# Kernel tuning notes

Hardware: AMD Instinct MI355X
Metric: run time of the kernel (lower is better)

Reference implementation:

```python
import jax, jax.numpy as jnp
import numpy as np
from jax import lax

B, N, S = 4, 16384, 4096
D1, D2 = 128, 256
MLP = (256, 128)
EPS_W = 1e-8
EPS_BN = 1e-5
BIG = 1e8


def setup_inputs() -> dict:
    key = jax.random.key(0)
    ks = jax.random.split(key, 10)
    inp = {
        "xyz1": jax.random.normal(ks[0], (B, 3, N), jnp.float32),
        "xyz2": jax.random.normal(ks[1], (B, 3, S), jnp.float32),
        "points1": jax.random.normal(ks[2], (B, D1, N), jnp.float32),
        "points2": jax.random.normal(ks[3], (B, D2, S), jnp.float32),
        "idx1": jnp.repeat(jnp.arange(B, dtype=jnp.int32), N).reshape(B, N),
        "idx2": jnp.repeat(jnp.arange(B, dtype=jnp.int32), S).reshape(B, S),
    }
    cin = D1 + D2
    inp["w1"] = jax.random.normal(ks[4], (MLP[0], cin), jnp.float32) * 0.05
    inp["b1"] = jnp.zeros((MLP[0],), jnp.float32)
    inp["g1"] = jnp.ones((MLP[0],), jnp.float32)
    inp["be1"] = jnp.zeros((MLP[0],), jnp.float32)
    inp["w2"] = jax.random.normal(ks[5], (MLP[1], MLP[0]), jnp.float32) * 0.05
    inp["b2"] = jnp.zeros((MLP[1],), jnp.float32)
    inp["g2"] = jnp.ones((MLP[1],), jnp.float32)
    inp["be2"] = jnp.zeros((MLP[1],), jnp.float32)
    return inp


def _bn_relu(x, gamma, beta):
    # training-mode batchnorm over (B, N) per channel, then relu; x: [B, C, N]
    mean = jnp.mean(x, axis=(0, 2), keepdims=True)
    var = jnp.var(x, axis=(0, 2), keepdims=True)  # biased, as torch BN
    xn = (x - mean) * lax.rsqrt(var + EPS_BN)
    return jax.nn.relu(xn * gamma[None, :, None] + beta[None, :, None])


def _fp_forward(xyz1, xyz2, points1, points2, idx1, idx2,
                w1, b1, g1, be1, w2, b2, g2, be2):
    x1 = jnp.transpose(xyz1, (0, 2, 1))  # [B, N, 3]
    x2 = jnp.transpose(xyz2, (0, 2, 1))  # [B, S, 3]
    p2 = jnp.transpose(points2, (0, 2, 1))  # [B, S, D2]

    # squared pairwise distances [B, N, S]
    d = -2.0 * jnp.einsum('bnc,bsc->bns', x1, x2)
    d = d + jnp.sum(x1 * x1, -1)[:, :, None] + jnp.sum(x2 * x2, -1)[:, None, :]
    d = jnp.where(idx1[:, :, None] == idx2[:, None, :], d, jnp.inf)

    # 3 nearest neighbors (top-k on negated distances == sort-ascending take 3)
    neg_d3, idx3 = lax.top_k(-d, 3)          # [B, N, 3]
    d3 = -neg_d3
    recip = 1.0 / (d3 + EPS_W)
    weight = recip / jnp.sum(recip, axis=2, keepdims=True)
    weight = jnp.where(d3 > BIG, 0.0, weight)
    weight = jnp.nan_to_num(weight)

    gathered = jax.vmap(lambda p, i: p[i])(p2, idx3)   # [B, N, 3, D2]
    interp = jnp.sum(gathered * weight[..., None], axis=2)  # [B, N, D2]

    newp = jnp.concatenate([jnp.transpose(points1, (0, 2, 1)), interp], axis=-1)
    newp = jnp.transpose(newp, (0, 2, 1))  # [B, D1+D2, N]

    # 1x1 conv -> BN -> relu, twice
    h = jnp.einsum('bcn,oc->bon', newp, w1) + b1[None, :, None]
    h = _bn_relu(h, g1, be1)
    h = jnp.einsum('bcn,oc->bon', h, w2) + b2[None, :, None]
    h = _bn_relu(h, g2, be2)
    return h


def reference(xyz1, xyz2, points1, points2, idx1, idx2,
              w1, b1, g1, be1, w2, b2, g2, be2):
    return _fp_forward(xyz1, xyz2, points1, points2, idx1, idx2,
                       w1, b1, g1, be1, w2, b2, g2, be2)
```

## Files before the change

kernel.cpp:

```cpp
#include <hip/hip_runtime.h>
#include <hip/hip_bf16.h>

#define INF_F (__builtin_inff())

typedef __attribute__((ext_vector_type(8))) short bf16x8;
typedef __attribute__((ext_vector_type(4))) float f32x4;

__device__ __forceinline__ unsigned short f2bf(float f) {
  __hip_bfloat16 h = __float2bfloat16(f);
  return __builtin_bit_cast(unsigned short, h);
}
__device__ __forceinline__ float bf2f(unsigned short u) {
  return __uint_as_float((unsigned)u << 16);
}

#define TOP3_INS(d, sj, E0, E1, E2, J0, J1, J2)                      \
  {                                                                  \
    bool l0 = (d) < E0, l1 = (d) < E1;                               \
    E2 = l1 ? E1 : (d); J2 = l1 ? J1 : (sj);                         \
    E1 = l0 ? E0 : (l1 ? (d) : E1); J1 = l0 ? J0 : (l1 ? (sj) : J1); \
    E0 = l0 ? (d) : E0; J0 = l0 ? (sj) : J0;                         \
  }


__global__ __launch_bounds__(256) void prep_k(const float* __restrict__ p2,
                                              const float* __restrict__ p1,
                                              const float* __restrict__ w1,
                                              const float* __restrict__ w2,
                                              const float* __restrict__ xyz2,
                                              const int* __restrict__ idx1,
                                              const int* __restrict__ idx2,
                                              unsigned short* __restrict__ p2t,
                                              unsigned short* __restrict__ X,
                                              unsigned short* __restrict__ w1b,
                                              unsigned short* __restrict__ w2b,
                                              float4* __restrict__ pack,
                                              float* __restrict__ stats) {
  int id = blockIdx.x;
  int t = threadIdx.x;
  if (id < 4096) {
    __shared__ float tile[32][33];
    int s0 = (id & 127) * 32;
    int k0 = ((id >> 7) & 7) * 32;
    int b = id >> 10;
    int tx = t & 31, ty = t >> 5;
    const float* src = p2 + ((size_t)b * 256 + k0) * 4096 + s0;
    for (int r = ty; r < 32; r += 8) tile[r][tx] = src[(size_t)r * 4096 + tx];
    __syncthreads();
    unsigned short* dst = p2t + ((size_t)b * 4096 + s0) * 256 + k0;
    for (int r = ty; r < 32; r += 8) dst[(size_t)r * 256 + tx] = f2bf(tile[tx][r]);
  } else if (id < 12288) {
    __shared__ float tile[32][33];
    int id2 = id - 4096;
    int n0 = (id2 & 511) * 32;
    int c0 = ((id2 >> 9) & 3) * 32;
    int b = id2 >> 11;
    int tx = t & 31, ty = t >> 5;
    const float* src = p1 + ((size_t)b * 128 + c0) * 16384 + n0;
    for (int r = ty; r < 32; r += 8) tile[r][tx] = src[(size_t)r * 16384 + tx];
    __syncthreads();
    for (int r = ty; r < 32; r += 8)
      X[((size_t)(b * 16384 + n0 + r)) * 384 + c0 + tx] = f2bf(tile[tx][r]);
  } else if (id < 12864) {
    int id3 = (id - 12288) * 256 + t;
    if (id3 < 98304) {
      w1b[id3] = f2bf(w1[id3]);
    } else if (id3 < 131072) {
      w2b[id3 - 98304] = f2bf(w2[id3 - 98304]);
    } else {
      int pid = id3 - 131072;
      int b = pid >> 12, s = pid & 4095;
      float x = xyz2[(b * 3 + 0) * 4096 + s];
      float y = xyz2[(b * 3 + 1) * 4096 + s];
      float z = xyz2[(b * 3 + 2) * 4096 + s];
      float w = fmaf(x, x, fmaf(y, y, z * z));
      int common = idx1[b * 16384];
      w = (idx2[b * 4096 + s] == common) ? w : 3e38f;
      pack[b * 4096 + s] = make_float4(x, y, z, w);
    }
  } else {
    for (int i = t; i < 768; i += 256) stats[i] = 0.f;
  }
}

__global__ __launch_bounds__(256) void knn_k(const float* __restrict__ xyz1,
                                             const float* __restrict__ xyz2,
                                             const int* __restrict__ idx1,
                                             const int* __restrict__ idx2,
                                             const float4* __restrict__ pack,
                                             float* __restrict__ rec) {
  int bid = blockIdx.x;
  int qg = bid >> 3, sl = bid & 7;
  int b = qg >> 6;
  int nloc = (qg & 63) << 8;
  int t = threadIdx.x;
  int n = nloc + t;
  int q0i = b * 16384 + n;
  int common = idx1[b * 16384];
  int sbase = sl << 9;
  const float4* ps = pack + b * 4096 + sbase;
  float px = xyz1[(b * 3 + 0) * 16384 + n];
  float py = xyz1[(b * 3 + 1) * 16384 + n];
  float pz = xyz1[(b * 3 + 2) * 16384 + n];
  int myid = idx1[q0i];
  float pn = fmaf(px, px, fmaf(py, py, pz * pz));
  float qx = -2.f * px, qy = -2.f * py, qz = -2.f * pz;
  float e0 = INF_F, e1 = INF_F, e2 = INF_F;
  int j0 = 0, j1 = 0, j2 = 0;
#pragma unroll 8
  for (int s = 0; s < 512; ++s) {
    float4 p = ps[s];
    float d = fmaf(qx, p.x, fmaf(qy, p.y, fmaf(qz, p.z, pn))) + p.w;
    if (__builtin_expect(d < e2, 0)) {
      int sj = sbase + s;
      TOP3_INS(d, sj, e0, e1, e2, j0, j1, j2);
    }
  }
  if (__builtin_expect(myid != common, 0)) {
    e0 = INF_F; e1 = INF_F; e2 = INF_F; j0 = 0; j1 = 0; j2 = 0;
    for (int s = 0; s < 512; ++s) {
      int gs = sbase + s;
      float x = xyz2[(b * 3 + 0) * 4096 + gs];
      float y = xyz2[(b * 3 + 1) * 4096 + gs];
      float z = xyz2[(b * 3 + 2) * 4096 + gs];
      float w = fmaf(x, x, fmaf(y, y, z * z));
      float d = fmaf(qx, x, fmaf(qy, y, fmaf(qz, z, pn))) + w;
      d = (idx2[b * 4096 + gs] == myid) ? d : INF_F;
      if (d < e2) TOP3_INS(d, gs, e0, e1, e2, j0, j1, j2);
    }
  }
  float* r = &rec[((size_t)sl * 65536 + q0i) * 6];
  r[0] = e0; r[1] = e1; r[2] = e2;
  ((int*)r)[3] = j0; ((int*)r)[4] = j1; ((int*)r)[5] = j2;
}

__global__ __launch_bounds__(256) void interpm_k(const float* __restrict__ rec,
                                                 const unsigned short* __restrict__ p2t,
                                                 unsigned short* __restrict__ X) {
  __shared__ int sId[128][3];
  __shared__ float sWt[128][3];
  int i0 = blockIdx.x * 128;
  int b = i0 >> 14;
  int t = threadIdx.x;
  if (t < 128) {
    int i = i0 + t;
    float e0, e1, e2;
    int j0, j1, j2;
    {
      const float* r = &rec[(size_t)i * 6];
      e0 = r[0]; e1 = r[1]; e2 = r[2];
      j0 = ((const int*)r)[3]; j1 = ((const int*)r)[4]; j2 = ((const int*)r)[5];
    }
#pragma unroll
    for (int c = 1; c < 8; ++c) {
      const float* r = &rec[((size_t)c * 65536 + i) * 6];
      const int* ir = (const int*)r;
#pragma unroll
      for (int w = 0; w < 3; ++w) {
        float d = r[w];
        int sj = ir[3 + w];
        bool l0 = (d < e0) || (d == e0 && sj < j0);
        bool l1 = (d < e1) || (d == e1 && sj < j1);
        bool l2 = (d < e2) || (d == e2 && sj < j2);
        e2 = l1 ? e1 : (l2 ? d : e2);
        j2 = l1 ? j1 : (l2 ? sj : j2);
        e1 = l0 ? e0 : (l1 ? d : e1);
        j1 = l0 ? j0 : (l1 ? sj : j1);
        e0 = l0 ? d : e0;
        j0 = l0 ? sj : j0;
      }
    }
    float r0 = 1.f / (e0 + 1e-8f);
    float r1 = 1.f / (e1 + 1e-8f);
    float r2 = 1.f / (e2 + 1e-8f);
    float rs = r0 + r1 + r2;
    sWt[t][0] = (e0 > 1e8f) ? 0.f : r0 / rs;
    sWt[t][1] = (e1 > 1e8f) ? 0.f : r1 / rs;
    sWt[t][2] = (e2 > 1e8f) ? 0.f : r2 / rs;
    sId[t][0] = j0; sId[t][1] = j1; sId[t][2] = j2;
  }
  __syncthreads();
  int k = t;
  const unsigned short* base = p2t + (size_t)b * 4096 * 256;
#pragma unroll 2
  for (int ii = 0; ii < 128; ++ii) {
    int id0 = sId[ii][0], id1 = sId[ii][1], id2 = sId[ii][2];
    float w0 = sWt[ii][0], w1v = sWt[ii][1], w2v = sWt[ii][2];
    float v = w0 * bf2f(base[id0 * 256 + k]);
    v = fmaf(w1v, bf2f(base[id1 * 256 + k]), v);
    v = fmaf(w2v, bf2f(base[id2 * 256 + k]), v);
    X[(size_t)(i0 + ii) * 384 + 128 + k] = f2bf(v);
  }
}

__global__ __launch_bounds__(256) void gemm1_k(const unsigned short* __restrict__ X,
                                               const unsigned short* __restrict__ Wb,
                                               unsigned short* __restrict__ h1T,
                                               float* __restrict__ stats1) {
  __shared__ unsigned short sW[128][40];
  __shared__ unsigned short sX[128][40];
  int t = threadIdx.x;
  int i0 = blockIdx.x * 128;
  int c0 = blockIdx.y * 128;
  int w = t >> 6, lane = t & 63;
  int wc = (w & 1) * 64, wni = w >> 1;
  int wn = wni * 64;
  int l15 = lane & 15, g = lane >> 4;
  f32x4 acc[4][4];
#pragma unroll
  for (int a = 0; a < 4; ++a)
#pragma unroll
    for (int bq = 0; bq < 4; ++bq) acc[a][bq] = (f32x4)0.f;
  int sr = t & 127, sh = t >> 7;
  for (int kc = 0; kc < 12; ++kc) {
    int k0 = kc * 32;
    __syncthreads();
    {
      const uint4* gw = (const uint4*)&Wb[(size_t)(c0 + sr) * 384 + k0 + sh * 16];
      uint4 v0 = gw[0], v1 = gw[1];
      *(uint4*)&sW[sr][sh * 16] = v0;
      *(uint4*)&sW[sr][sh * 16 + 8] = v1;
      const uint4* gx = (const uint4*)&X[(size_t)(i0 + sr) * 384 + k0 + sh * 16];
      uint4 x0 = gx[0], x1 = gx[1];
      *(uint4*)&sX[sr][sh * 16] = x0;
      *(uint4*)&sX[sr][sh * 16 + 8] = x1;
    }
    __syncthreads();
    bf16x8 a[4], b[4];
#pragma unroll
    for (int tm = 0; tm < 4; ++tm)
      a[tm] = *(const bf16x8*)&sW[wc + tm * 16 + l15][g * 8];
#pragma unroll
    for (int tn = 0; tn < 4; ++tn)
      b[tn] = *(const bf16x8*)&sX[wn + tn * 16 + l15][g * 8];
#pragma unroll
    for (int tm = 0; tm < 4; ++tm)
#pragma unroll
      for (int tn = 0; tn < 4; ++tn)
        acc[tm][tn] = __builtin_amdgcn_mfma_f32_16x16x32_bf16(a[tm], b[tn], acc[tm][tn], 0, 0, 0);
  }
#pragma unroll
  for (int tm = 0; tm < 4; ++tm)
#pragma unroll
    for (int tn = 0; tn < 4; ++tn) {
      int c = c0 + wc + tm * 16 + g * 4;
      int n = i0 + wn + tn * 16 + l15;
      f32x4 v = acc[tm][tn];
      ushort4 o;
      o.x = f2bf(v[0]); o.y = f2bf(v[1]); o.z = f2bf(v[2]); o.w = f2bf(v[3]);
      *(ushort4*)&h1T[(size_t)n * 256 + c] = o;
    }
  float s_[4][4], q_[4][4];
#pragma unroll
  for (int tm = 0; tm < 4; ++tm)
#pragma unroll
    for (int j = 0; j < 4; ++j) {
      float s = 0.f, q = 0.f;
#pragma unroll
      for (int tn = 0; tn < 4; ++tn) {
        float v = acc[tm][tn][j];
        s += v; q = fmaf(v, v, q);
      }
      s_[tm][j] = s; q_[tm][j] = q;
    }
#pragma unroll
  for (int mask = 1; mask < 16; mask <<= 1)
#pragma unroll
    for (int tm = 0; tm < 4; ++tm)
#pragma unroll
      for (int j = 0; j < 4; ++j) {
        s_[tm][j] += __shfl_xor(s_[tm][j], mask);
        q_[tm][j] += __shfl_xor(q_[tm][j], mask);
      }
  __syncthreads();
  float* red = (float*)&sW[0][0];
  if (l15 == 0) {
#pragma unroll
    for (int tm = 0; tm < 4; ++tm)
#pragma unroll
      for (int j = 0; j < 4; ++j) {
        int cl = wc + tm * 16 + g * 4 + j;
        red[(wni * 128 + cl) * 2 + 0] = s_[tm][j];
        red[(wni * 128 + cl) * 2 + 1] = q_[tm][j];
      }
  }
  __syncthreads();
  {
    int cl = t >> 1, st = t & 1;
    float v = red[(0 * 128 + cl) * 2 + st] + red[(1 * 128 + cl) * 2 + st];
    atomicAdd(&stats1[((c0 + cl) << 1) + st], v);
  }
}

__global__ __launch_bounds__(256) void gemm2_k(const unsigned short* __restrict__ h1T,
                                               const unsigned short* __restrict__ Wb,
                                               const float* __restrict__ stats1,
                                               const float* __restrict__ g1,
                                               const float* __restrict__ be1,
                                               unsigned short* __restrict__ o2,
                                               float* __restrict__ stats2) {
  __shared__ unsigned short sW[128][40];
  __shared__ unsigned short sX[128][40];
  __shared__ float sA1[256], sC1[256];
  int t = threadIdx.x;
  int i0 = blockIdx.x * 128;
  int w = t >> 6, lane = t & 63;
  int wc = (w & 1) * 64, wni = w >> 1;
  int wn = wni * 64;
  int l15 = lane & 15, g = lane >> 4;
  {
    float s1v = stats1[t * 2 + 0], s2v = stats1[t * 2 + 1];
    float mean = s1v * (1.f / 65536.f);
    float var = s2v * (1.f / 65536.f) - mean * mean;
    float a = g1[t] * rsqrtf(var + 1e-5f);
    sA1[t] = a;
    sC1[t] = be1[t] - mean * a;
  }
  f32x4 acc[4][4];
#pragma unroll
  for (int a = 0; a < 4; ++a)
#pragma unroll
    for (int bq = 0; bq < 4; ++bq) acc[a][bq] = (f32x4)0.f;
  int sr = t & 127, sh = t >> 7;
  for (int kc = 0; kc < 8; ++kc) {
    int k0 = kc * 32;
    int kcol = k0 + sh * 16;
    __syncthreads();
    {
      const uint4* gw = (const uint4*)&Wb[(size_t)sr * 256 + kcol];
      uint4 v0 = gw[0], v1 = gw[1];
      *(uint4*)&sW[sr][sh * 16] = v0;
      *(uint4*)&sW[sr][sh * 16 + 8] = v1;
      const uint4* gx = (const uint4*)&h1T[(size_t)(i0 + sr) * 256 + kcol];
      uint4 x0 = gx[0], x1 = gx[1];
      unsigned rr[8] = {x0.x, x0.y, x0.z, x0.w, x1.x, x1.y, x1.z, x1.w};
      unsigned ww[8];
#pragma unroll
      for (int e = 0; e < 8; ++e) {
        int ch = kcol + 2 * e;
        float f0 = bf2f((unsigned short)(rr[e] & 0xFFFFu));
        float f1 = bf2f((unsigned short)(rr[e] >> 16));
        f0 = fmaxf(fmaf(sA1[ch], f0, sC1[ch]), 0.f);
        f1 = fmaxf(fmaf(sA1[ch + 1], f1, sC1[ch + 1]), 0.f);
        ww[e] = (unsigned)f2bf(f0) | ((unsigned)f2bf(f1) << 16);
      }
      uint4 y0 = {ww[0], ww[1], ww[2], ww[3]};
      uint4 y1 = {ww[4], ww[5], ww[6], ww[7]};
      *(uint4*)&sX[sr][sh * 16] = y0;
      *(uint4*)&sX[sr][sh * 16 + 8] = y1;
    }
    __syncthreads();
    bf16x8 a[4], b[4];
#pragma unroll
    for (int tm = 0; tm < 4; ++tm)
      a[tm] = *(const bf16x8*)&sW[wc + tm * 16 + l15][g * 8];
#pragma unroll
    for (int tn = 0; tn < 4; ++tn)
      b[tn] = *(const bf16x8*)&sX[wn + tn * 16 + l15][g * 8];
#pragma unroll
    for (int tm = 0; tm < 4; ++tm)
#pragma unroll
      for (int tn = 0; tn < 4; ++tn)
        acc[tm][tn] = __builtin_amdgcn_mfma_f32_16x16x32_bf16(a[tm], b[tn], acc[tm][tn], 0, 0, 0);
  }
#pragma unroll
  for (int tm = 0; tm < 4; ++tm)
#pragma unroll
    for (int tn = 0; tn < 4; ++tn) {
      int c = wc + tm * 16 + g * 4;
      int n = i0 + wn + tn * 16 + l15;
      f32x4 v = acc[tm][tn];
      ushort4 o;
      o.x = f2bf(v[0]); o.y = f2bf(v[1]); o.z = f2bf(v[2]); o.w = f2bf(v[3]);
      *(ushort4*)&o2[(size_t)n * 128 + c] = o;
    }
  float s_[4][4], q_[4][4];
#pragma unroll
  for (int tm = 0; tm < 4; ++tm)
#pragma unroll
    for (int j = 0; j < 4; ++j) {
      float s = 0.f, q = 0.f;
#pragma unroll
      for (int tn = 0; tn < 4; ++tn) {
        float v = acc[tm][tn][j];
        s += v; q = fmaf(v, v, q);
      }
      s_[tm][j] = s; q_[tm][j] = q;
    }
#pragma unroll
  for (int mask = 1; mask < 16; mask <<= 1)
#pragma unroll
    for (int tm = 0; tm < 4; ++tm)
#pragma unroll
      for (int j = 0; j < 4; ++j) {
        s_[tm][j] += __shfl_xor(s_[tm][j], mask);
        q_[tm][j] += __shfl_xor(q_[tm][j], mask);
      }
  __syncthreads();
  float* red = (float*)&sW[0][0];
  if (l15 == 0) {
#pragma unroll
    for (int tm = 0; tm < 4; ++tm)
#pragma unroll
      for (int j = 0; j < 4; ++j) {
        int cl = wc + tm * 16 + g * 4 + j;
        red[(wni * 128 + cl) * 2 + 0] = s_[tm][j];
        red[(wni * 128 + cl) * 2 + 1] = q_[tm][j];
      }
  }
  __syncthreads();
  {
    int cl = t >> 1, st = t & 1;
    float v = red[(0 * 128 + cl) * 2 + st] + red[(1 * 128 + cl) * 2 + st];
    atomicAdd(&stats2[(cl << 1) + st], v);
  }
}

__global__ __launch_bounds__(256) void final_k(const unsigned short* __restrict__ o2,
                                               const float* __restrict__ stats2,
                                               const float* __restrict__ g2,
                                               const float* __restrict__ be2,
                                               float* __restrict__ out) {
  __shared__ float tile[32][33];
  __shared__ float sA2[128], sC2[128];
  int b = blockIdx.z;
  int n0 = blockIdx.x * 32;
  int c0 = blockIdx.y * 32;
  int tx = threadIdx.x, ty = threadIdx.y;
  int tid = ty * 32 + tx;
  if (tid < 128) {
    float s1v = stats2[tid * 2 + 0], s2v = stats2[tid * 2 + 1];
    float mean = s1v * (1.f / 65536.f);
    float var = s2v * (1.f / 65536.f) - mean * mean;
    float a = g2[tid] * rsqrtf(var + 1e-5f);
    sA2[tid] = a;
    sC2[tid] = be2[tid] - mean * a;
  }
  __syncthreads();
  float a = sA2[c0 + tx], cc = sC2[c0 + tx];
  for (int r = ty; r < 32; r += 8) {
    float v = bf2f(o2[(size_t)(b * 16384 + n0 + r) * 128 + c0 + tx]);
    tile[r][tx] = fmaxf(fmaf(a, v, cc), 0.f);
  }
  __syncthreads();
  for (int r = ty; r < 32; r += 8)
    out[((size_t)(b * 128 + c0 + r)) * 16384 + n0 + tx] = tile[tx][r];
}

extern "C" void kernel_launch(void* const* d_in, const int* in_sizes, int n_in,
                              void* d_out, int out_size, void* d_ws, size_t ws_size,
                              hipStream_t stream) {
  const float* xyz1 = (const float*)d_in[0];
  const float* xyz2 = (const float*)d_in[1];
  const float* p1   = (const float*)d_in[2];
  const float* p2   = (const float*)d_in[3];
  const int*   idx1 = (const int*)d_in[4];
  const int*   idx2 = (const int*)d_in[5];
  const float* w1   = (const float*)d_in[6];
  const float* g1   = (const float*)d_in[8];
  const float* be1  = (const float*)d_in[9];
  const float* w2   = (const float*)d_in[10];
  const float* g2   = (const float*)d_in[12];
  const float* be2  = (const float*)d_in[13];
  float* out = (float*)d_out;

  char* ws = (char*)d_ws;
  unsigned short* X    = (unsigned short*)(ws + 0x180000);
  unsigned short* h1T  = (unsigned short*)(ws + 0x3180000);
  unsigned short* p2t  = (unsigned short*)(ws + 0x3180000);
  unsigned short* o2   = (unsigned short*)(ws + 0x5180000);
  float*          rec  = (float*)(ws + 0x5180000);
  unsigned short* w1b  = (unsigned short*)(ws + 0x7180000);
  unsigned short* w2b  = (unsigned short*)(ws + 0x71B0000);
  float4*         pack = (float4*)(ws + 0x71C0000);
  float*          stats = (float*)(ws + 0x7208000);
  float*          stats1 = stats;
  float*          stats2 = stats + 512;

  hipLaunchKernelGGL(prep_k, dim3(12865), dim3(256), 0, stream,
                     p2, p1, w1, w2, xyz2, idx1, idx2, p2t, X, w1b, w2b, pack, stats);
  hipLaunchKernelGGL(knn_k, dim3(2048), dim3(256), 0, stream,
                     xyz1, xyz2, idx1, idx2, pack, rec);
  hipLaunchKernelGGL(interpm_k, dim3(512), dim3(256), 0, stream, rec, p2t, X);
  hipLaunchKernelGGL(gemm1_k, dim3(512, 2), dim3(256), 0, stream, X, w1b, h1T, stats1);
  hipLaunchKernelGGL(gemm2_k, dim3(512), dim3(256), 0, stream,
                     h1T, w2b, stats1, g1, be1, o2, stats2);
  hipLaunchKernelGGL(final_k, dim3(512, 4, 4), dim3(32, 8), 0, stream,
                     o2, stats2, g2, be2, out);
}
```

Before: 233.7 us.

## Fuse transpose/convert prep work into the KNN kernel, split out small pack kernel

The bf16 transposes of points1/points2 and the weight conversions move out of the large prep kernel and into the KNN kernel, which is compute-bound, so the memory traffic can overlap with the distance search. A small separate kernel now builds the xyz2 pack and zeroes the stats. Each KNN block handles two p2 tiles and four p1 tiles before its search loop, which adds syncthreads and shared-memory use to that kernel and may lower its occupancy.

After: 233.7 us. About the same (-0.0%).

```diff
diff --git a/kernel.cpp b/kernel.cpp
--- a/kernel.cpp
+++ b/kernel.cpp
@@ -23,77 +23,80 @@
   }
 
 
-__global__ __launch_bounds__(256) void prep_k(const float* __restrict__ p2,
-                                              const float* __restrict__ p1,
-                                              const float* __restrict__ w1,
-                                              const float* __restrict__ w2,
-                                              const float* __restrict__ xyz2,
+__global__ __launch_bounds__(256) void pack_k(const float* __restrict__ xyz2,
                                               const int* __restrict__ idx1,
                                               const int* __restrict__ idx2,
-                                              unsigned short* __restrict__ p2t,
-                                              unsigned short* __restrict__ X,
-                                              unsigned short* __restrict__ w1b,
-                                              unsigned short* __restrict__ w2b,
                                               float4* __restrict__ pack,
                                               float* __restrict__ stats) {
   int id = blockIdx.x;
   int t = threadIdx.x;
-  if (id < 4096) {
-    __shared__ float tile[32][33];
+  if (id < 64) {
+    int pid = id * 256 + t;
+    int b = pid >> 12, s = pid & 4095;
+    float x = xyz2[(b * 3 + 0) * 4096 + s];
+    float y = xyz2[(b * 3 + 1) * 4096 + s];
+    float z = xyz2[(b * 3 + 2) * 4096 + s];
+    float w = fmaf(x, x, fmaf(y, y, z * z));
+    int common = idx1[b * 16384];
+    w = (idx2[b * 4096 + s] == common) ? w : 3e38f;
+    pack[b * 4096 + s] = make_float4(x, y, z, w);
+  } else {
+    for (int i = t; i < 768; i += 256) stats[i] = 0.f;
+  }
+}
+
+__global__ __launch_bounds__(256) void knnprep_k(const float* __restrict__ xyz1,
+                                                 const float* __restrict__ xyz2,
+                                                 const int* __restrict__ idx1,
+                                                 const int* __restrict__ idx2,
+                                                 const float4* __restrict__ pack,
+                                                 const float* __restrict__ p2,
+                                                 const float* __restrict__ p1,
+                                                 const float* __restrict__ w1,
+                                                 const float* __restrict__ w2,
+                                                 unsigned short* __restrict__ p2t,
+                                                 unsigned short* __restrict__ X,
+                                                 unsigned short* __restrict__ w1b,
+                                                 unsigned short* __restrict__ w2b,
+                                                 float* __restrict__ rec) {
+  __shared__ float tile[32][33];
+  int bid = blockIdx.x;
+  int t = threadIdx.x;
+  int tx = t & 31, ty = t >> 5;
+  if (bid < 512) {
+    int id3 = bid * 256 + t;
+    if (id3 < 98304) w1b[id3] = f2bf(w1[id3]);
+    else w2b[id3 - 98304] = f2bf(w2[id3 - 98304]);
+  }
+#pragma unroll
+  for (int q = 0; q < 2; ++q) {
+    int id = bid * 2 + q;
     int s0 = (id & 127) * 32;
     int k0 = ((id >> 7) & 7) * 32;
     int b = id >> 10;
-    int tx = t & 31, ty = t >> 5;
     const float* src = p2 + ((size_t)b * 256 + k0) * 4096 + s0;
+    __syncthreads();
     for (int r = ty; r < 32; r += 8) tile[r][tx] = src[(size_t)r * 4096 + tx];
     __syncthreads();
     unsigned short* dst = p2t + ((size_t)b * 4096 + s0) * 256 + k0;
     for (int r = ty; r < 32; r += 8) dst[(size_t)r * 256 + tx] = f2bf(tile[tx][r]);
-  } else if (id < 12288) {
-    __shared__ float tile[32][33];
-    int id2 = id - 4096;
+  }
+#pragma unroll
+  for (int q = 0; q < 4; ++q) {
+    int id2 = bid * 4 + q;
     int n0 = (id2 & 511) * 32;
     int c0 = ((id2 >> 9) & 3) * 32;
     int b = id2 >> 11;
-    int tx = t & 31, ty = t >> 5;
     const float* src = p1 + ((size_t)b * 128 + c0) * 16384 + n0;
+    __syncthreads();
     for (int r = ty; r < 32; r += 8) tile[r][tx] = src[(size_t)r * 16384 + tx];
     __syncthreads();
     for (int r = ty; r < 32; r += 8)
       X[((size_t)(b * 16384 + n0 + r)) * 384 + c0 + tx] = f2bf(tile[tx][r]);
-  } else if (id < 12864) {
-    int id3 = (id - 12288) * 256 + t;
-    if (id3 < 98304) {
-      w1b[id3] = f2bf(w1[id3]);
-    } else if (id3 < 131072) {
-      w2b[id3 - 98304] = f2bf(w2[id3 - 98304]);
-    } else {
-      int pid = id3 - 131072;
-      int b = pid >> 12, s = pid & 4095;
-      float x = xyz2[(b * 3 + 0) * 4096 + s];
-      float y = xyz2[(b * 3 + 1) * 4096 + s];
-      float z = xyz2[(b * 3 + 2) * 4096 + s];
-      float w = fmaf(x, x, fmaf(y, y, z * z));
-      int common = idx1[b * 16384];
-      w = (idx2[b * 4096 + s] == common) ? w : 3e38f;
-      pack[b * 4096 + s] = make_float4(x, y, z, w);
-    }
-  } else {
-    for (int i = t; i < 768; i += 256) stats[i] = 0.f;
-  }
-}
-
-__global__ __launch_bounds__(256) void knn_k(const float* __restrict__ xyz1,
-                                             const float* __restrict__ xyz2,
-                                             const int* __restrict__ idx1,
-                                             const int* __restrict__ idx2,
-                                             const float4* __restrict__ pack,
-                                             float* __restrict__ rec) {
-  int bid = blockIdx.x;
+  }
   int qg = bid >> 3, sl = bid & 7;
   int b = qg >> 6;
   int nloc = (qg & 63) << 8;
-  int t = threadIdx.x;
   int n = nloc + t;
   int q0i = b * 16384 + n;
   int common = idx1[b * 16384];
@@ -477,10 +480,11 @@
   float*          stats1 = stats;
   float*          stats2 = stats + 512;
 
-  hipLaunchKernelGGL(prep_k, dim3(12865), dim3(256), 0, stream,
-                     p2, p1, w1, w2, xyz2, idx1, idx2, p2t, X, w1b, w2b, pack, stats);
-  hipLaunchKernelGGL(knn_k, dim3(2048), dim3(256), 0, stream,
-                     xyz1, xyz2, idx1, idx2, pack, rec);
+  hipLaunchKernelGGL(pack_k, dim3(65), dim3(256), 0, stream,
+                     xyz2, idx1, idx2, pack, stats);
+  hipLaunchKernelGGL(knnprep_k, dim3(2048), dim3(256), 0, stream,
+                     xyz1, xyz2, idx1, idx2, pack, p2, p1, w1, w2,
+                     p2t, X, w1b, w2b, rec);
   hipLaunchKernelGGL(interpm_k, dim3(512), dim3(256), 0, stream, rec, p2t, X);
   hipLaunchKernelGGL(gemm1_k, dim3(512, 2), dim3(256), 0, stream, X, w1b, h1T, stats1);
   hipLaunchKernelGGL(gemm2_k, dim3(512), dim3(256), 0, stream,
```
